# Optimization experiments

Measured on AMD Instinct MI355X. Metric: run time of the kernel, lower is better.

## Reference

```python
import jax, jax.numpy as jnp
from jax import lax
import numpy as np

B, A, C, H, W = 256, 64, 8, 15, 15
E = 128
CONV_CH = [8, 16, 32, 16, 32]   # in -> hidden[16,32,16] -> out(32)
FLAT = 32 * 7 * 7               # four 3x3 VALID convs: 15 -> 7
MLP_DIMS = [FLAT, 128, 128, 128]


def setup_inputs() -> dict:
    key = jax.random.key(0)
    ks = jax.random.split(key, 16)
    inp = {}
    inp["states"] = jax.random.normal(ks[0], (B, A, C, H, W), jnp.float32)
    # nonnegative weighted adjacency (dense graph, diagonal included like the
    # original loop which always appends (i,i) with weight adj[b,i,i])
    inp["adjacencies"] = jax.random.uniform(ks[1], (B, A, A), jnp.float32)
    for l, (ci, co) in enumerate(zip(CONV_CH[:-1], CONV_CH[1:])):
        inp[f"cw{l}"] = jax.random.normal(ks[2 + l], (co, ci, 3, 3), jnp.float32) * 0.05
        inp[f"cb{l}"] = jnp.zeros((co,), jnp.float32)
    for l, (di, do) in enumerate(zip(MLP_DIMS[:-1], MLP_DIMS[1:])):
        inp[f"mw{l}"] = jax.random.normal(ks[8 + l], (di, do), jnp.float32) * 0.02
        inp[f"mb{l}"] = jnp.zeros((do,), jnp.float32)
    inp["gw"] = jax.random.normal(ks[12], (E, E), jnp.float32) * 0.05
    inp["gb"] = jnp.zeros((E,), jnp.float32)
    return inp


def _conv(x, w, b):
    y = lax.conv_general_dilated(x, w, (1, 1), "VALID",
                                 dimension_numbers=("NCHW", "OIHW", "NCHW"))
    return jax.nn.relu(y + b[None, :, None, None])


def reference(states, adjacencies, cw0, cb0, cw1, cb1, cw2, cb2, cw3, cb3,
              mw0, mb0, mw1, mb1, mw2, mb2, gw, gb):
    b, a, c, h, w = states.shape
    x = states.reshape(b * a, c, h, w)
    # CNN encoder (batched over all B*A agent observations at once)
    for cw, cb in ((cw0, cb0), (cw1, cb1), (cw2, cb2), (cw3, cb3)):
        x = _conv(x, cw, cb)
    x = x.reshape(b * a, -1)
    # MLP: relu on hidden layers, linear output
    x = jax.nn.relu(x @ mw0 + mb0)
    x = jax.nn.relu(x @ mw1 + mb1)
    feats = x @ mw2 + mb2                      # [B*A, E]
    feats = feats.reshape(b, a, E)
    # GCNConv(add_self_loops=False): out = D^{-1/2} A D^{-1/2} aggregation
    # edge (i,j): row=source i, col=target j; deg from target (column sums)
    xw = jnp.einsum("bae,ef->baf", feats, gw)  # x @ W
    deg = adjacencies.sum(axis=1)              # deg[b,j] = sum_i A[b,i,j]
    dinv = jnp.where(deg > 0, 1.0 / jnp.sqrt(jnp.where(deg > 0, deg, 1.0)), 0.0)
    norm = dinv[:, :, None] * adjacencies * dinv[:, None, :]  # N[b,i,j]
    out = jnp.einsum("bij,bie->bje", norm, xw) + gb            # out[b,j] = sum_i N_ij xW_i
    return out.reshape(b * a, E)
```

## Files before the change

### kernel.cpp

```cpp
#include <hip/hip_runtime.h>


typedef short short8 __attribute__((ext_vector_type(8)));
typedef float f32x4  __attribute__((ext_vector_type(4)));

__device__ __forceinline__ unsigned short f2bf(float f) {
    unsigned u = __builtin_bit_cast(unsigned, f);
    u = (u + 0x7FFFu + ((u >> 16) & 1u)) >> 16;
    return (unsigned short)u;
}
__device__ __forceinline__ float bf2f(unsigned short h) {
    unsigned u = ((unsigned)h) << 16;
    return __builtin_bit_cast(float, u);
}

#define ZED_OFF 26304
#define ARENA_FLOATS 6592

__global__ __launch_bounds__(256) void wprep(
    const float* __restrict__ cw0, const float* __restrict__ cw1,
    const float* __restrict__ cw2, const float* __restrict__ cw3,
    short* __restrict__ wbuf)
{
    int gidx = blockIdx.x * 256 + threadIdx.x;
    if (gidx >= 36864) return;
    const float* cw; int base, CI, NM, KIND;
    if (gidx < 3072)       { cw = cw0; base = 0;     CI = 8;  NM = 1; KIND = 0; }
    else if (gidx < 15360) { cw = cw1; base = 3072;  CI = 16; NM = 2; KIND = 1; }
    else if (gidx < 24576) { cw = cw2; base = 15360; CI = 32; NM = 1; KIND = 2; }
    else                   { cw = cw3; base = 24576; CI = 16; NM = 2; KIND = 1; }
    int e = gidx - base;
    int j = e & 7, lane = (e >> 3) & 63, rest = e >> 9;
    int comp = rest & 1, cm = rest >> 1;
    int m = cm % NM, c = cm / NM;
    int g = lane >> 4, colr = lane & 15;
    int co = m * 16 + colr;
    int ky, kx, ci; bool pad = false;
    if (KIND == 0)      { ky = c; kx = g; ci = j; pad = (g >= 3); }
    else if (KIND == 1) {
        ky = c >> 1; int half = c & 1;
        if (half == 0) { kx = g >> 1; ci = (g & 1) * 8 + j; }
        else           { kx = 2;      ci = (g & 1) * 8 + j; pad = (g >= 2); }
    } else              { ky = c / 3; kx = c % 3; ci = g * 8 + j; }
    float w = pad ? 0.0f : cw[((co * CI + ci) * 3 + ky) * 3 + kx];
    unsigned short h = f2bf(w);
    wbuf[gidx] = (comp == 0) ? (short)h : (short)f2bf(w - bf2f(h));
}

template<int CI, int CO, int WIN, int WOUT, int POUT, int NM, int NT,
         int KIND, int INOFF, int DIN, int OUTOFF, int DOUT, int GOUT>
__device__ __forceinline__ void mfma_layer(
    float* __restrict__ A, const short* __restrict__ wbuf,
    const float* __restrict__ bias, float* __restrict__ gOut, int tid)
{
    const char* Ac = (const char*)A;
    char* Aw = (char*)A;
    const int wv = tid >> 6, lane = tid & 63;
    const int g = lane >> 4, col = lane & 15;
    constexpr int UNITS = NT * NM;
    constexpr int CPK = (KIND == 0) ? 1 : (KIND == 1) ? 2 : 3;
    constexpr int KB = WIN * CI * 2;
    const int u0 = (UNITS * wv) >> 2, u1 = (UNITS * (wv + 1)) >> 2;

#pragma unroll 1
    for (int u = u0; u < u1; ++u) {
        const int n = u / NM, m = u - n * NM;
        const int p = n * 16 + col;
        const bool valid = (p < POUT);
        const int pix = valid ? p : (POUT - 1);
        const int y = pix / WOUT;
        const int x = pix - y * WOUT;
        const int ob = INOFF + (y * WIN + x) * (CI * 2);
        const int vbF = ob + g * 16;
        const int vbH = ob + (g & 1) * 16;
        const bool fOK = (KIND == 0) ? (g < 3) : true;
        const bool hOK = (g < 2);

        f32x4 acc;
        {
            const float4 bv = *(const float4*)(bias + m * 16 + g * 4);
            acc[0] = bv.x; acc[1] = bv.y; acc[2] = bv.z; acc[3] = bv.w;
        }

#pragma unroll
        for (int ky = 0; ky < 3; ++ky) {
#pragma unroll
            for (int cc = 0; cc < CPK; ++cc) {
                const int c = ky * CPK + cc;
                const int koff = ky * KB +
                    ((KIND == 2) ? cc * (CI * 2) : (cc == 1 ? 2 * (CI * 2) : 0));
                const bool okv = (KIND == 0) ? fOK
                               : ((KIND == 1 && cc == 1) ? hOK : true);
                const int vb = (KIND == 1 && cc == 1) ? vbH : vbF;
                const int vH = okv ? (vb + koff) : ZED_OFF;
                const int vL = okv ? (vb + koff + DIN) : ZED_OFF;

                const short8 Ah = *(const short8*)(
                    wbuf + ((c * NM + m) * 2 + 0) * 512 + lane * 8);
                const short8 Al = *(const short8*)(
                    wbuf + ((c * NM + m) * 2 + 1) * 512 + lane * 8);

                const short8 Bh = *(const short8*)(Ac + vH);
                acc = __builtin_amdgcn_mfma_f32_16x16x32_bf16(Ah, Bh, acc, 0, 0, 0);
                acc = __builtin_amdgcn_mfma_f32_16x16x32_bf16(Al, Bh, acc, 0, 0, 0);
                const short8 Bl = *(const short8*)(Ac + vL);
                acc = __builtin_amdgcn_mfma_f32_16x16x32_bf16(Ah, Bl, acc, 0, 0, 0);
            }
        }

        if (GOUT) {
            if (valid) {
                const int co0 = m * 16 + g * 4;
#pragma unroll
                for (int r = 0; r < 4; ++r)
                    gOut[(co0 + r) * POUT + pix] = fmaxf(acc[r], 0.0f);
            }
        } else if (valid) {
            unsigned hh[2], ll[2];
#pragma unroll
            for (int r2 = 0; r2 < 2; ++r2) {
                float v0 = fmaxf(acc[r2 * 2 + 0], 0.0f);
                float v1 = fmaxf(acc[r2 * 2 + 1], 0.0f);
                unsigned short h0 = f2bf(v0), h1 = f2bf(v1);
                unsigned short l0 = f2bf(v0 - bf2f(h0));
                unsigned short l1 = f2bf(v1 - bf2f(h1));
                hh[r2] = (unsigned)h0 | ((unsigned)h1 << 16);
                ll[r2] = (unsigned)l0 | ((unsigned)l1 << 16);
            }
            const int ob2 = OUTOFF + (pix * CO + m * 16 + g * 4) * 2;
            *(uint2*)(Aw + ob2)        = make_uint2(hh[0], hh[1]);
            *(uint2*)(Aw + ob2 + DOUT) = make_uint2(ll[0], ll[1]);
        }
    }
}

__global__ __launch_bounds__(256) void conv_mfma(
    const float* __restrict__ states, const short* __restrict__ wbuf,
    const float* __restrict__ cb0, const float* __restrict__ cb1,
    const float* __restrict__ cb2, const float* __restrict__ cb3,
    float* __restrict__ x0out)
{
    __shared__ float A[ARENA_FLOATS];
    const int tid = threadIdx.x;

    if (tid < 4) A[ZED_OFF / 4 + tid] = 0.0f;

    const float* gin = states + (size_t)blockIdx.x * 1800;
    {
        char* Aw = (char*)A;
#pragma unroll
        for (int it = 0; it < 8; ++it) {
            int e = tid + it * 256;
            if (e < 1800) {
                float f = gin[e];
                int ci = e / 225, p = e - ci * 225;
                unsigned short h = f2bf(f);
                unsigned short l = f2bf(f - bf2f(h));
                int off = 10816 + (p * 8 + ci) * 2;
                *(short*)(Aw + off) = (short)h;
                *(short*)(Aw + off + 3600) = (short)l;
            }
        }
    }
    __syncthreads();

    mfma_layer<8, 16, 15, 13, 169, 1, 11, 0, 10816, 3600, 0, 5408, 0>(
        A, wbuf + 0, cb0, nullptr, tid);
    __syncthreads();
    mfma_layer<16, 32, 13, 11, 121, 2, 8, 1, 0, 5408, 10816, 7744, 0>(
        A, wbuf + 3072, cb1, nullptr, tid);
    __syncthreads();
    mfma_layer<32, 16, 11, 9, 81, 1, 6, 2, 10816, 7744, 0, 2592, 0>(
        A, wbuf + 15360, cb2, nullptr, tid);
    __syncthreads();
    float* gOut = x0out + (size_t)blockIdx.x * 1568;
    mfma_layer<16, 32, 9, 7, 49, 2, 4, 1, 0, 2592, 0, 0, 1>(
        A, wbuf + 24576, cb3, gOut, tid);
}

template<int K, bool RELU>
__global__ __launch_bounds__(256) void gemm128(
    const float* __restrict__ Am, const float* __restrict__ Wm,
    const float* __restrict__ bias, float* __restrict__ Cm)
{
    __shared__ float As[64 * 36];
    __shared__ float Ws[32 * 128];

    const int tid = threadIdx.x;
    const int m0  = blockIdx.x * 64;
    const int rg  = tid >> 4;
    const int cg  = tid & 15;

    float acc[4][8];
#pragma unroll
    for (int r = 0; r < 4; r++)
#pragma unroll
        for (int c = 0; c < 8; c++) acc[r][c] = 0.0f;

    for (int k0 = 0; k0 < K; k0 += 32) {
        __syncthreads();
#pragma unroll
        for (int it = 0; it < 2; it++) {
            int idx = tid + it * 256;
            int row = idx >> 3;
            int c4  = idx & 7;
            float4 v = *(const float4*)(Am + (size_t)(m0 + row) * K + k0 + c4 * 4);
            *(float4*)(As + row * 36 + c4 * 4) = v;
        }
#pragma unroll
        for (int it = 0; it < 4; it++) {
            int idx = tid + it * 256;
            int kr  = idx >> 5;
            int c4  = idx & 31;
            float4 v = *(const float4*)(Wm + (size_t)(k0 + kr) * 128 + c4 * 4);
            *(float4*)(Ws + kr * 128 + c4 * 4) = v;
        }
        __syncthreads();

#pragma unroll
        for (int kk = 0; kk < 32; kk++) {
            float a0 = As[(rg * 4 + 0) * 36 + kk];
            float a1 = As[(rg * 4 + 1) * 36 + kk];
            float a2 = As[(rg * 4 + 2) * 36 + kk];
            float a3 = As[(rg * 4 + 3) * 36 + kk];
            float4 w0 = *(const float4*)(Ws + kk * 128 + cg * 8);
            float4 w1 = *(const float4*)(Ws + kk * 128 + cg * 8 + 4);
            acc[0][0] += a0 * w0.x; acc[0][1] += a0 * w0.y; acc[0][2] += a0 * w0.z; acc[0][3] += a0 * w0.w;
            acc[0][4] += a0 * w1.x; acc[0][5] += a0 * w1.y; acc[0][6] += a0 * w1.z; acc[0][7] += a0 * w1.w;
            acc[1][0] += a1 * w0.x; acc[1][1] += a1 * w0.y; acc[1][2] += a1 * w0.z; acc[1][3] += a1 * w0.w;
            acc[1][4] += a1 * w1.x; acc[1][5] += a1 * w1.y; acc[1][6] += a1 * w1.z; acc[1][7] += a1 * w1.w;
            acc[2][0] += a2 * w0.x; acc[2][1] += a2 * w0.y; acc[2][2] += a2 * w0.z; acc[2][3] += a2 * w0.w;
            acc[2][4] += a2 * w1.x; acc[2][5] += a2 * w1.y; acc[2][6] += a2 * w1.z; acc[2][7] += a2 * w1.w;
            acc[3][0] += a3 * w0.x; acc[3][1] += a3 * w0.y; acc[3][2] += a3 * w0.z; acc[3][3] += a3 * w0.w;
            acc[3][4] += a3 * w1.x; acc[3][5] += a3 * w1.y; acc[3][6] += a3 * w1.z; acc[3][7] += a3 * w1.w;
        }
    }

#pragma unroll
    for (int r = 0; r < 4; r++) {
        int row = m0 + rg * 4 + r;
        float v[8];
#pragma unroll
        for (int c = 0; c < 8; c++) {
            float x = acc[r][c];
            if (bias) x += bias[cg * 8 + c];
            if (RELU) x = fmaxf(x, 0.0f);
            v[c] = x;
        }
        float* gp = Cm + (size_t)row * 128 + cg * 8;
        *(float4*)(gp)     = make_float4(v[0], v[1], v[2], v[3]);
        *(float4*)(gp + 4) = make_float4(v[4], v[5], v[6], v[7]);
    }
}

__global__ __launch_bounds__(256) void gcn_agg(
    const float* __restrict__ adj, const float* __restrict__ xw,
    const float* __restrict__ gb, float* __restrict__ outp)
{
    __shared__ float sAdj[64 * 64];
    __shared__ float sXW[64 * 128];
    __shared__ float sDinv[64];

    const int b = blockIdx.x;
    const int tid = threadIdx.x;

    const float* ga = adj + (size_t)b * 4096;
#pragma unroll
    for (int it = 0; it < 4; it++) {
        int idx = tid + it * 256;
        *(float4*)(sAdj + idx * 4) = *(const float4*)(ga + idx * 4);
    }
    const float* gx = xw + (size_t)b * 8192;
#pragma unroll
    for (int it = 0; it < 8; it++) {
        int idx = tid + it * 256;
        *(float4*)(sXW + idx * 4) = *(const float4*)(gx + idx * 4);
    }
    __syncthreads();

    if (tid < 64) {
        float d = 0.0f;
        for (int i = 0; i < 64; i++) d += sAdj[i * 64 + tid];
        sDinv[tid] = (d > 0.0f) ? rsqrtf(d) : 0.0f;
    }
    __syncthreads();

#pragma unroll
    for (int it = 0; it < 8; it++) {
        int idx = tid + it * 256;
        int i = idx >> 5;
        float s = sDinv[i];
        float4 v = *(float4*)(sXW + idx * 4);
        v.x *= s; v.y *= s; v.z *= s; v.w *= s;
        *(float4*)(sXW + idx * 4) = v;
    }
    __syncthreads();

    const int j  = tid >> 2;
    const int eb = (tid & 3) * 32;
    float acc[32];
#pragma unroll
    for (int e = 0; e < 32; e++) acc[e] = 0.0f;

    for (int i = 0; i < 64; i++) {
        float wgt = sAdj[i * 64 + j];
        const float* xp = sXW + i * 128 + eb;
#pragma unroll
        for (int e4 = 0; e4 < 8; e4++) {
            float4 v = *(const float4*)(xp + e4 * 4);
            acc[e4 * 4 + 0] += wgt * v.x;
            acc[e4 * 4 + 1] += wgt * v.y;
            acc[e4 * 4 + 2] += wgt * v.z;
            acc[e4 * 4 + 3] += wgt * v.w;
        }
    }

    const float dj = sDinv[j];
    float* go = outp + ((size_t)b * 64 + j) * 128 + eb;
#pragma unroll
    for (int e4 = 0; e4 < 8; e4++) {
        float4 v;
        v.x = acc[e4 * 4 + 0] * dj + gb[eb + e4 * 4 + 0];
        v.y = acc[e4 * 4 + 1] * dj + gb[eb + e4 * 4 + 1];
        v.z = acc[e4 * 4 + 2] * dj + gb[eb + e4 * 4 + 2];
        v.w = acc[e4 * 4 + 3] * dj + gb[eb + e4 * 4 + 3];
        *(float4*)(go + e4 * 4) = v;
    }
}

extern "C" void kernel_launch(void* const* d_in, const int* in_sizes, int n_in,
                              void* d_out, int out_size, void* d_ws, size_t ws_size,
                              hipStream_t stream)
{
    const float* states = (const float*)d_in[0];
    const float* adj    = (const float*)d_in[1];
    const float* cw0 = (const float*)d_in[2];  const float* cb0 = (const float*)d_in[3];
    const float* cw1 = (const float*)d_in[4];  const float* cb1 = (const float*)d_in[5];
    const float* cw2 = (const float*)d_in[6];  const float* cb2 = (const float*)d_in[7];
    const float* cw3 = (const float*)d_in[8];  const float* cb3 = (const float*)d_in[9];
    const float* mw0 = (const float*)d_in[10]; const float* mb0 = (const float*)d_in[11];
    const float* mw1 = (const float*)d_in[12]; const float* mb1 = (const float*)d_in[13];
    const float* mw2 = (const float*)d_in[14]; const float* mb2 = (const float*)d_in[15];
    const float* gw  = (const float*)d_in[16]; const float* gb  = (const float*)d_in[17];

    float* ws = (float*)d_ws;
    float* X0 = ws;
    float* Bu = ws + (size_t)25690112;
    float* Cu = Bu + (size_t)2097152;
    short* WB = (short*)(Cu + (size_t)2097152);

    float* out = (float*)d_out;

    wprep<<<144, 256, 0, stream>>>(cw0, cw1, cw2, cw3, WB);
    conv_mfma<<<16384, 256, 0, stream>>>(states, WB, cb0, cb1, cb2, cb3, X0);
    gemm128<1568, true ><<<256, 256, 0, stream>>>(X0, mw0, mb0, Bu);
    gemm128<128,  true ><<<256, 256, 0, stream>>>(Bu, mw1, mb1, Cu);
    gemm128<128,  false><<<256, 256, 0, stream>>>(Cu, mw2, mb2, Bu);
    gemm128<128,  false><<<256, 256, 0, stream>>>(Bu, gw, nullptr, Cu);
    gcn_agg<<<256, 256, 0, stream>>>(adj, Cu, gb, out);
}
```

Measured before the change: 651.6 us.

## Move MLP GEMMs to split-bf16 MFMA and re-layout conv LDS as channel-group planes

```diff
diff --git a/kernel.cpp b/kernel.cpp
--- a/kernel.cpp
+++ b/kernel.cpp
@@ -47,11 +47,35 @@
     wbuf[gidx] = (comp == 0) ? (short)h : (short)f2bf(w - bf2f(h));
 }
 
+__global__ __launch_bounds__(256) void wprep_mlp(
+    const float* __restrict__ mw0, const float* __restrict__ mw1,
+    const float* __restrict__ mw2, const float* __restrict__ gw,
+    short* __restrict__ wp)
+{
+    int gidx = blockIdx.x * 256 + threadIdx.x;
+    if (gidx >= 499712) return;
+    const float* W; int base;
+    if (gidx < 401408)      { W = mw0; base = 0; }
+    else if (gidx < 434176) { W = mw1; base = 401408; }
+    else if (gidx < 466944) { W = mw2; base = 434176; }
+    else                    { W = gw;  base = 466944; }
+    int e = gidx - base;
+    int j = e & 7, lane = (e >> 3) & 63, rest = e >> 9;
+    int comp = rest & 1, knn = rest >> 1;
+    int nn = knn & 7, kc = knn >> 3;
+    int k = kc * 32 + (lane >> 4) * 8 + j;
+    int n = nn * 16 + (lane & 15);
+    float w = W[(size_t)k * 128 + n];
+    unsigned short h = f2bf(w);
+    wp[gidx] = (comp == 0) ? (short)h : (short)f2bf(w - bf2f(h));
+}
+
 template<int CI, int CO, int WIN, int WOUT, int POUT, int NM, int NT,
-         int KIND, int INOFF, int DIN, int OUTOFF, int DOUT, int GOUT>
+         int KIND, int INOFF, int NPIN, int OUTOFF, int GOUT>
 __device__ __forceinline__ void mfma_layer(
     float* __restrict__ A, const short* __restrict__ wbuf,
-    const float* __restrict__ bias, float* __restrict__ gOut, int tid)
+    const float* __restrict__ bias, short* __restrict__ gH,
+    short* __restrict__ gL, int tid)
 {
     const char* Ac = (const char*)A;
     char* Aw = (char*)A;
@@ -59,7 +83,8 @@
     const int g = lane >> 4, col = lane & 15;
     constexpr int UNITS = NT * NM;
     constexpr int CPK = (KIND == 0) ? 1 : (KIND == 1) ? 2 : 3;
-    constexpr int KB = WIN * CI * 2;
+    constexpr int DIN = (CI / 8) * NPIN * 16;
+    constexpr int DOUT = (CO / 8) * POUT * 16;
     const int u0 = (UNITS * wv) >> 2, u1 = (UNITS * (wv + 1)) >> 2;
 
 #pragma unroll 1
@@ -70,11 +95,6 @@
         const int pix = valid ? p : (POUT - 1);
         const int y = pix / WOUT;
         const int x = pix - y * WOUT;
-        const int ob = INOFF + (y * WIN + x) * (CI * 2);
-        const int vbF = ob + g * 16;
-        const int vbH = ob + (g & 1) * 16;
-        const bool fOK = (KIND == 0) ? (g < 3) : true;
-        const bool hOK = (g < 2);
 
         f32x4 acc;
         {
@@ -86,14 +106,16 @@
         for (int ky = 0; ky < 3; ++ky) {
 #pragma unroll
             for (int cc = 0; cc < CPK; ++cc) {
+                int kg, kx; bool okv;
+                if (KIND == 0)      { kx = g;      kg = 0;     okv = (g < 3); }
+                else if (KIND == 1) {
+                    if (cc == 0)    { kx = g >> 1; kg = g & 1; okv = true; }
+                    else            { kx = 2;      kg = g & 1; okv = (g < 2); }
+                } else              { kx = cc;     kg = g;     okv = true; }
+                const int pin = (y + ky) * WIN + x + kx;
+                const int vH = okv ? (INOFF + (kg * NPIN + pin) * 16) : ZED_OFF;
+                const int vL = okv ? (vH + DIN) : ZED_OFF;
                 const int c = ky * CPK + cc;
-                const int koff = ky * KB +
-                    ((KIND == 2) ? cc * (CI * 2) : (cc == 1 ? 2 * (CI * 2) : 0));
-                const bool okv = (KIND == 0) ? fOK
-                               : ((KIND == 1 && cc == 1) ? hOK : true);
-                const int vb = (KIND == 1 && cc == 1) ? vbH : vbF;
-                const int vH = okv ? (vb + koff) : ZED_OFF;
-                const int vL = okv ? (vb + koff + DIN) : ZED_OFF;
 
                 const short8 Ah = *(const short8*)(
                     wbuf + ((c * NM + m) * 2 + 0) * 512 + lane * 8);
@@ -112,8 +134,12 @@
             if (valid) {
                 const int co0 = m * 16 + g * 4;
 #pragma unroll
-                for (int r = 0; r < 4; ++r)
-                    gOut[(co0 + r) * POUT + pix] = fmaxf(acc[r], 0.0f);
+                for (int r = 0; r < 4; ++r) {
+                    float v = fmaxf(acc[r], 0.0f);
+                    unsigned short h = f2bf(v);
+                    gH[(co0 + r) * POUT + pix] = (short)h;
+                    gL[(co0 + r) * POUT + pix] = (short)f2bf(v - bf2f(h));
+                }
             }
         } else if (valid) {
             unsigned hh[2], ll[2];
@@ -127,7 +153,8 @@
                 hh[r2] = (unsigned)h0 | ((unsigned)h1 << 16);
                 ll[r2] = (unsigned)l0 | ((unsigned)l1 << 16);
             }
-            const int ob2 = OUTOFF + (pix * CO + m * 16 + g * 4) * 2;
+            const int kgO = m * 2 + (g >> 1);
+            const int ob2 = OUTOFF + (kgO * POUT + pix) * 16 + (g & 1) * 8;
             *(uint2*)(Aw + ob2)        = make_uint2(hh[0], hh[1]);
             *(uint2*)(Aw + ob2 + DOUT) = make_uint2(ll[0], ll[1]);
         }
@@ -138,7 +165,7 @@
     const float* __restrict__ states, const short* __restrict__ wbuf,
     const float* __restrict__ cb0, const float* __restrict__ cb1,
     const float* __restrict__ cb2, const float* __restrict__ cb3,
-    float* __restrict__ x0out)
+    short* __restrict__ x0h, short* __restrict__ x0l)
 {
     __shared__ float A[ARENA_FLOATS];
     const int tid = threadIdx.x;
@@ -156,7 +183,7 @@
                 int ci = e / 225, p = e - ci * 225;
                 unsigned short h = f2bf(f);
                 unsigned short l = f2bf(f - bf2f(h));
-                int off = 10816 + (p * 8 + ci) * 2;
+                int off = 10816 + p * 16 + ci * 2;
                 *(short*)(Aw + off) = (short)h;
                 *(short*)(Aw + off + 3600) = (short)l;
             }
@@ -164,92 +191,70 @@
     }
     __syncthreads();
 
-    mfma_layer<8, 16, 15, 13, 169, 1, 11, 0, 10816, 3600, 0, 5408, 0>(
-        A, wbuf + 0, cb0, nullptr, tid);
-    __syncthreads();
-    mfma_layer<16, 32, 13, 11, 121, 2, 8, 1, 0, 5408, 10816, 7744, 0>(
-        A, wbuf + 3072, cb1, nullptr, tid);
-    __syncthreads();
-    mfma_layer<32, 16, 11, 9, 81, 1, 6, 2, 10816, 7744, 0, 2592, 0>(
-        A, wbuf + 15360, cb2, nullptr, tid);
-    __syncthreads();
-    float* gOut = x0out + (size_t)blockIdx.x * 1568;
-    mfma_layer<16, 32, 9, 7, 49, 2, 4, 1, 0, 2592, 0, 0, 1>(
-        A, wbuf + 24576, cb3, gOut, tid);
-}
-
-template<int K, bool RELU>
-__global__ __launch_bounds__(256) void gemm128(
-    const float* __restrict__ Am, const float* __restrict__ Wm,
-    const float* __restrict__ bias, float* __restrict__ Cm)
-{
-    __shared__ float As[64 * 36];
-    __shared__ float Ws[32 * 128];
-
+    mfma_layer<8, 16, 15, 13, 169, 1, 11, 0, 10816, 225, 0, 0>(
+        A, wbuf + 0, cb0, nullptr, nullptr, tid);
+    __syncthreads();
+    mfma_layer<16, 32, 13, 11, 121, 2, 8, 1, 0, 169, 10816, 0>(
+        A, wbuf + 3072, cb1, nullptr, nullptr, tid);
+    __syncthreads();
+    mfma_layer<32, 16, 11, 9, 81, 1, 6, 2, 10816, 121, 0, 0>(
+        A, wbuf + 15360, cb2, nullptr, nullptr, tid);
+    __syncthreads();
+    mfma_layer<16, 32, 9, 7, 49, 2, 4, 1, 0, 81, 0, 1>(
+        A, wbuf + 24576, cb3,
+        x0h + (size_t)blockIdx.x * 1568, x0l + (size_t)blockIdx.x * 1568, tid);
+}
+
+template<int KCH, bool RELU, bool OUTF32>
+__global__ __launch_bounds__(256) void mgemm(
+    const short* __restrict__ Ah, const short* __restrict__ Al,
+    const short* __restrict__ wp, const float* __restrict__ bias,
+    short* __restrict__ Ch, short* __restrict__ Cl, float* __restrict__ Cf)
+{
+    constexpr int K = KCH * 32;
     const int tid = threadIdx.x;
-    const int m0  = blockIdx.x * 64;
-    const int rg  = tid >> 4;
-    const int cg  = tid & 15;
-
-    float acc[4][8];
-#pragma unroll
-    for (int r = 0; r < 4; r++)
-#pragma unroll
-        for (int c = 0; c < 8; c++) acc[r][c] = 0.0f;
-
-    for (int k0 = 0; k0 < K; k0 += 32) {
-        __syncthreads();
-#pragma unroll
-        for (int it = 0; it < 2; it++) {
-            int idx = tid + it * 256;
-            int row = idx >> 3;
-            int c4  = idx & 7;
-            float4 v = *(const float4*)(Am + (size_t)(m0 + row) * K + k0 + c4 * 4);
-            *(float4*)(As + row * 36 + c4 * 4) = v;
-        }
-#pragma unroll
-        for (int it = 0; it < 4; it++) {
-            int idx = tid + it * 256;
-            int kr  = idx >> 5;
-            int c4  = idx & 31;
-            float4 v = *(const float4*)(Wm + (size_t)(k0 + kr) * 128 + c4 * 4);
-            *(float4*)(Ws + kr * 128 + c4 * 4) = v;
-        }
-        __syncthreads();
-
-#pragma unroll
-        for (int kk = 0; kk < 32; kk++) {
-            float a0 = As[(rg * 4 + 0) * 36 + kk];
-            float a1 = As[(rg * 4 + 1) * 36 + kk];
-            float a2 = As[(rg * 4 + 2) * 36 + kk];
-            float a3 = As[(rg * 4 + 3) * 36 + kk];
-            float4 w0 = *(const float4*)(Ws + kk * 128 + cg * 8);
-            float4 w1 = *(const float4*)(Ws + kk * 128 + cg * 8 + 4);
-            acc[0][0] += a0 * w0.x; acc[0][1] += a0 * w0.y; acc[0][2] += a0 * w0.z; acc[0][3] += a0 * w0.w;
-            acc[0][4] += a0 * w1.x; acc[0][5] += a0 * w1.y; acc[0][6] += a0 * w1.z; acc[0][7] += a0 * w1.w;
-            acc[1][0] += a1 * w0.x; acc[1][1] += a1 * w0.y; acc[1][2] += a1 * w0.z; acc[1][3] += a1 * w0.w;
-            acc[1][4] += a1 * w1.x; acc[1][5] += a1 * w1.y; acc[1][6] += a1 * w1.z; acc[1][7] += a1 * w1.w;
-            acc[2][0] += a2 * w0.x; acc[2][1] += a2 * w0.y; acc[2][2] += a2 * w0.z; acc[2][3] += a2 * w0.w;
-            acc[2][4] += a2 * w1.x; acc[2][5] += a2 * w1.y; acc[2][6] += a2 * w1.z; acc[2][7] += a2 * w1.w;
-            acc[3][0] += a3 * w0.x; acc[3][1] += a3 * w0.y; acc[3][2] += a3 * w0.z; acc[3][3] += a3 * w0.w;
-            acc[3][4] += a3 * w1.x; acc[3][5] += a3 * w1.y; acc[3][6] += a3 * w1.z; acc[3][7] += a3 * w1.w;
-        }
-    }
-
-#pragma unroll
-    for (int r = 0; r < 4; r++) {
-        int row = m0 + rg * 4 + r;
-        float v[8];
-#pragma unroll
-        for (int c = 0; c < 8; c++) {
-            float x = acc[r][c];
-            if (bias) x += bias[cg * 8 + c];
-            if (RELU) x = fmaxf(x, 0.0f);
-            v[c] = x;
-        }
-        float* gp = Cm + (size_t)row * 128 + cg * 8;
-        *(float4*)(gp)     = make_float4(v[0], v[1], v[2], v[3]);
-        *(float4*)(gp + 4) = make_float4(v[4], v[5], v[6], v[7]);
+    const int wv = tid >> 6, lane = tid & 63;
+    const int col = lane & 15, g = lane >> 4;
+    const int row0 = blockIdx.x * 64 + wv * 16;
+    const size_t aoff = (size_t)(row0 + col) * K + g * 8;
+
+    f32x4 acc[8];
+#pragma unroll
+    for (int nn = 0; nn < 8; ++nn) {
+        float b = bias ? bias[nn * 16 + col] : 0.0f;
+        acc[nn][0] = b; acc[nn][1] = b; acc[nn][2] = b; acc[nn][3] = b;
+    }
+
+#pragma unroll 2
+    for (int kc = 0; kc < KCH; ++kc) {
+        const short8 fAh = *(const short8*)(Ah + aoff + kc * 32);
+        const short8 fAl = *(const short8*)(Al + aoff + kc * 32);
+        const short* wk = wp + (size_t)kc * 8192 + lane * 8;
+#pragma unroll
+        for (int nn = 0; nn < 8; ++nn) {
+            const short8 Bh = *(const short8*)(wk + (nn * 2 + 0) * 512);
+            const short8 Bl = *(const short8*)(wk + (nn * 2 + 1) * 512);
+            acc[nn] = __builtin_amdgcn_mfma_f32_16x16x32_bf16(fAh, Bh, acc[nn], 0, 0, 0);
+            acc[nn] = __builtin_amdgcn_mfma_f32_16x16x32_bf16(fAl, Bh, acc[nn], 0, 0, 0);
+            acc[nn] = __builtin_amdgcn_mfma_f32_16x16x32_bf16(fAh, Bl, acc[nn], 0, 0, 0);
+        }
+    }
+
+#pragma unroll
+    for (int nn = 0; nn < 8; ++nn) {
+#pragma unroll
+        for (int r = 0; r < 4; ++r) {
+            float v = acc[nn][r];
+            if (RELU) v = fmaxf(v, 0.0f);
+            const size_t idx = (size_t)(row0 + g * 4 + r) * 128 + nn * 16 + col;
+            if (OUTF32) {
+                Cf[idx] = v;
+            } else {
+                unsigned short h = f2bf(v);
+                Ch[idx] = (short)h;
+                Cl[idx] = (short)f2bf(v - bf2f(h));
+            }
+        }
     }
 }
 
@@ -344,18 +349,33 @@
     const float* gw  = (const float*)d_in[16]; const float* gb  = (const float*)d_in[17];
 
     float* ws = (float*)d_ws;
-    float* X0 = ws;
-    float* Bu = ws + (size_t)25690112;
-    float* Cu = Bu + (size_t)2097152;
-    short* WB = (short*)(Cu + (size_t)2097152);
+    const size_t X0E = (size_t)16384 * 1568;
+
+    short* X0h = (short*)ws;
+    short* X0l = X0h + X0E;
+    short* H1h = (short*)(ws + X0E);
+    short* H1l = H1h + 2097152;
+    short* H2h = (short*)(ws + X0E + 2097152);
+    short* H2l = H2h + 2097152;
+    short* WBc = (short*)(ws + X0E + 2 * 2097152);
+    short* WPm = WBc + 36864;
+    short* Fh = (short*)ws;
+    short* Fl = Fh + 2097152;
+    float* xw = ws + 2097152;
 
     float* out = (float*)d_out;
 
-    wprep<<<144, 256, 0, stream>>>(cw0, cw1, cw2, cw3, WB);
-    conv_mfma<<<16384, 256, 0, stream>>>(states, WB, cb0, cb1, cb2, cb3, X0);
-    gemm128<1568, true ><<<256, 256, 0, stream>>>(X0, mw0, mb0, Bu);
-    gemm128<128,  true ><<<256, 256, 0, stream>>>(Bu, mw1, mb1, Cu);
-    gemm128<128,  false><<<256, 256, 0, stream>>>(Cu, mw2, mb2, Bu);
-    gemm128<128,  false><<<256, 256, 0, stream>>>(Bu, gw, nullptr, Cu);
-    gcn_agg<<<256, 256, 0, stream>>>(adj, Cu, gb, out);
-}
+    wprep<<<144, 256, 0, stream>>>(cw0, cw1, cw2, cw3, WBc);
+    wprep_mlp<<<1952, 256, 0, stream>>>(mw0, mw1, mw2, gw, WPm);
+    conv_mfma<<<16384, 256, 0, stream>>>(states, WBc, cb0, cb1, cb2, cb3,
+                                         X0h, X0l);
+    mgemm<49, true,  false><<<256, 256, 0, stream>>>(X0h, X0l, WPm + 0,
+                                                     mb0, H1h, H1l, nullptr);
+    mgemm<4,  true,  false><<<256, 256, 0, stream>>>(H1h, H1l, WPm + 401408,
+                                                     mb1, H2h, H2l, nullptr);
+    mgemm<4,  false, false><<<256, 256, 0, stream>>>(H2h, H2l, WPm + 434176,
+                                                     mb2, Fh, Fl, nullptr);
+    mgemm<4,  false, true ><<<256, 256, 0, stream>>>(Fh, Fl, WPm + 466944,
+                                                     nullptr, nullptr, nullptr, xw);
+    gcn_agg<<<256, 256, 0, stream>>>(adj, xw, gb, out);
+}
```

After: 676.2 us. 1.04x slower.
